# Kernel optimization log

Measured on AMD Instinct MI355X. Metric: run time of the kernel, lower is better.

Reference implementation:

```python
import jax, jax.numpy as jnp
import numpy as np

B, N, D, H = 4, 1024, 1024, 16
DH = D // H  # head dim = 64
SCALE = D ** (-0.5)  # scale_with_head=False -> dim**-0.5


def setup_inputs() -> dict:
    key = jax.random.key(0)
    ks = jax.random.split(key, 6)
    x = jax.random.normal(ks[0], (B, N, D), dtype=jnp.float32)
    mask = jax.random.randint(ks[1], (B, N - 1), 0, 2).astype(bool)
    Wqkv = jax.random.normal(ks[2], (D, 3 * D), dtype=jnp.float32) * (D ** -0.5)
    bqkv = jax.random.normal(ks[3], (3 * D,), dtype=jnp.float32) * 0.02
    Wout = jax.random.normal(ks[4], (D, D), dtype=jnp.float32) * (D ** -0.5)
    bout = jax.random.normal(ks[5], (D,), dtype=jnp.float32) * 0.02
    return {"x": x, "mask": mask, "Wqkv": Wqkv, "bqkv": bqkv, "Wout": Wout, "bout": bout}


def reference(x, mask, Wqkv, bqkv, Wout, bout):
    b, n, _ = x.shape
    qkv = x @ Wqkv + bqkv                      # [b, n, 3D]
    q, k, v = jnp.split(qkv, 3, axis=-1)
    split_heads = lambda t: t.reshape(b, n, H, DH).transpose(0, 2, 1, 3)  # [b,h,n,d]
    q, k, v = split_heads(q), split_heads(k), split_heads(v)
    dots = jnp.einsum('bhid,bhjd->bhij', q, k) * SCALE  # [b,h,n,n]
    mask_value = -jnp.finfo(dots.dtype).max
    # F.pad(mask.flatten(1), (1,0), value=True): prepend one True column
    m = jnp.concatenate([jnp.ones((b, 1), dtype=bool), mask], axis=1)  # [b, n]
    pair = m[:, None, :] & m[:, :, None]       # [b, n, n]
    dots = jnp.where(pair[:, None, :, :], dots, mask_value)
    attn = jax.nn.softmax(dots, axis=-1)
    out = jnp.einsum('bhij,bhjd->bhid', attn, v)
    out = out.transpose(0, 2, 1, 3).reshape(b, n, D)
    out = out @ Wout + bout                    # dropout p=0.0 -> identity
    return (out, attn)
```

## Files before the change

kernel.cpp:

```cpp
#include <hip/hip_runtime.h>
#include <stdint.h>

#define DEV static __device__ __forceinline__

typedef __attribute__((ext_vector_type(8))) __bf16 bfx8;
typedef __attribute__((ext_vector_type(4))) float f32x4;

DEV short f2bfbits(float f) {
  union { float f; unsigned u; } v; v.f = f;
  unsigned r = v.u + 0x7fffu + ((v.u >> 16) & 1u);
  return (short)(r >> 16);
}

DEV void gload_lds16(const void* g, void* lds) {
  __builtin_amdgcn_global_load_lds(
      (const __attribute__((address_space(1))) void*)g,
      (__attribute__((address_space(3))) void*)lds, 16, 0, 0);
}

__global__ void k_prep(const float* __restrict__ x, short* __restrict__ xb,
                       const int* __restrict__ mask, unsigned char* __restrict__ msk,
                       const float* __restrict__ Wqkv, short* __restrict__ wqkvT,
                       const float* __restrict__ Wout, short* __restrict__ woutT) {
  __shared__ float tile[32][33];
  int bx = blockIdx.x;
  int t = threadIdx.x;
  if (bx < 4096) {
    int i = bx * 256 + t;
    float4 v = ((const float4*)x)[i];
    union { short s[4]; uint64_t u; } o;
    o.s[0] = f2bfbits(v.x); o.s[1] = f2bfbits(v.y);
    o.s[2] = f2bfbits(v.z); o.s[3] = f2bfbits(v.w);
    ((uint64_t*)xb)[i] = o.u;
  } else if (bx < 4112) {
    int i = (bx - 4096) * 256 + t;
    int b = i >> 10, n = i & 1023;
    msk[i] = (n == 0) ? (unsigned char)1 : (unsigned char)(mask[b * 1023 + n - 1] != 0);
  } else {
    int tb = bx - 4112;
    int bxx = tb & 127, byy = tb >> 7;
    const float* src; short* dst; int C;
    if (bxx < 96) { src = Wqkv; dst = wqkvT; C = 3072; }
    else          { src = Wout; dst = woutT; C = 1024; bxx -= 96; }
    const int R = 1024;
    int c0 = bxx * 32, r0 = byy * 32;
    int tx = t & 31, ty = t >> 5;
    #pragma unroll
    for (int j = 0; j < 32; j += 8)
      tile[ty + j][tx] = src[(size_t)(r0 + ty + j) * C + c0 + tx];
    __syncthreads();
    #pragma unroll
    for (int j = 0; j < 32; j += 8)
      dst[(size_t)(c0 + ty + j) * R + r0 + tx] = f2bfbits(tile[tx][ty + j]);
  }
}

__global__ __launch_bounds__(256)
void k_gemm(const short* __restrict__ A, const short* __restrict__ Bt,
            const float* __restrict__ bias, int K,
            short* __restrict__ qf, short* __restrict__ kf,
            short* __restrict__ vf) {
  __shared__ short smem[8192];
  short* As = smem;
  short* Bs = smem + 4096;
  const int t = threadIdx.x;
  const int l = t & 63, w = t >> 6;
  const int lr = l & 15, lk = l >> 4;
  const int m0 = blockIdx.y * 128, n0 = blockIdx.x * 128;
  const int wr = (w >> 1) * 64, wc = (w & 1) * 64;
  f32x4 acc[4][4] = {};

  const int srow = t >> 2;
  const int sc8 = (t & 3) * 8;
  const size_t aoff1 = (size_t)(m0 + srow) * K + sc8;
  const size_t aoff2 = (size_t)(m0 + srow + 64) * K + sc8;
  const size_t boff1 = (size_t)(n0 + srow) * K + sc8;
  const size_t boff2 = (size_t)(n0 + srow + 64) * K + sc8;
  short* asd1 = As + (t & ~63) * 8;
  short* asd2 = As + (t & ~63) * 8 + 2048;
  short* bsd1 = Bs + (t & ~63) * 8;
  short* bsd2 = Bs + (t & ~63) * 8 + 2048;

  for (int k0 = 0; k0 < K; k0 += 32) {
    gload_lds16(A + aoff1 + k0, asd1);
    gload_lds16(A + aoff2 + k0, asd2);
    gload_lds16(Bt + boff1 + k0, bsd1);
    gload_lds16(Bt + boff2 + k0, bsd2);
    __syncthreads();
    bfx8 af[4], bf[4];
    #pragma unroll
    for (int m = 0; m < 4; m++)
      af[m] = *(const bfx8*)&As[(wr + m * 16 + lr) * 32 + lk * 8];
    #pragma unroll
    for (int n = 0; n < 4; n++)
      bf[n] = *(const bfx8*)&Bs[(wc + n * 16 + lr) * 32 + lk * 8];
    #pragma unroll
    for (int m = 0; m < 4; m++)
      #pragma unroll
      for (int n = 0; n < 4; n++)
        acc[m][n] = __builtin_amdgcn_mfma_f32_16x16x32_bf16(af[m], bf[n], acc[m][n], 0, 0, 0);
    __syncthreads();
  }

  const int which = n0 >> 10;
  const int head = w & 1;
  const int band = w >> 1;
  const int bb = m0 >> 10;
  const int bh = bb * 16 + ((n0 & 1023) >> 6) + head;
  short* dstp = (which == 0) ? qf : (which == 1) ? kf : vf;

  #pragma unroll
  for (int p = 0; p < 2; p++) {
    #pragma unroll
    for (int mm = 0; mm < 2; mm++) {
      int m = 2 * p + mm;
      #pragma unroll
      for (int n = 0; n < 4; n++) {
        int gc = n0 + wc + n * 16 + lr;
        float bv = bias[gc];
        #pragma unroll
        for (int i = 0; i < 4; i++) {
          short val = f2bfbits(acc[m][n][i] + bv);
          int off;
          if (which < 2) {
            off = ((((band * 2 + head) * 2 + mm) * 2 + (n >> 1)) * 64 +
                   ((2 * n + (lr >> 3)) & 3) * 16 + 4 * lk + i) * 8 + (lr & 7);
          } else {
            off = (((band * 2 + head) * 4 + n) * 64 +
                   (2 * mm + ((4 * lk + i) >> 3)) * 16 + lr) * 8 + ((4 * lk + i) & 7);
          }
          smem[off] = val;
        }
      }
    }
    __syncthreads();
    if (which < 2) {
      #pragma unroll
      for (int r = 0; r < 4; r++) {
        int rb = r >> 1, rh = r & 1;
        int bh_r = bb * 16 + ((n0 & 1023) >> 6) + rh;
        int blk0 = ((m0 & 1023) >> 4) + 4 * rb + 2 * p;
        size_t g = ((size_t)(bh_r * 64 + blk0) << 10) + t * 8;
        *(int4*)&dstp[g] = *(const int4*)&smem[r * 2048 + t * 8];
      }
    } else {
      #pragma unroll
      for (int r = 0; r < 4; r++) {
        int rb = r >> 1, rh = r & 1;
        int bh_r = bb * 16 + ((n0 & 1023) >> 6) + rh;
        int jj = ((m0 & 1023) >> 5) + 2 * rb + p;
        int db = t >> 6;
        size_t g = (((size_t)(bh_r * 4 + db) * 32 + jj) << 9) + (t & 63) * 8;
        *(int4*)&dstp[g] = *(const int4*)&smem[r * 2048 + t * 8];
      }
    }
    if (p == 0) __syncthreads();
  }
}

__global__ __launch_bounds__(256)
void k_gemm_out(const short* __restrict__ A, const short* __restrict__ Bt,
                const float* __restrict__ bias, float* __restrict__ outF) {
  __shared__ short As[128 * 32];
  __shared__ short Bs[64 * 32];
  const int K = 1024;
  const int t = threadIdx.x;
  const int l = t & 63, w = t >> 6;
  const int lr = l & 15, lk = l >> 4;
  const int m0 = blockIdx.y * 128, n0 = blockIdx.x * 64;
  const int wr = (w >> 1) * 64, wc = (w & 1) * 32;
  f32x4 acc[4][2] = {};

  const int srow = t >> 2;
  const int sc8 = (t & 3) * 8;
  const size_t aoff1 = (size_t)(m0 + srow) * K + sc8;
  const size_t aoff2 = (size_t)(m0 + srow + 64) * K + sc8;
  const size_t boff1 = (size_t)(n0 + srow) * K + sc8;
  short* asd1 = As + (t & ~63) * 8;
  short* asd2 = As + (t & ~63) * 8 + 2048;
  short* bsd1 = Bs + (t & ~63) * 8;

  for (int k0 = 0; k0 < K; k0 += 32) {
    gload_lds16(A + aoff1 + k0, asd1);
    gload_lds16(A + aoff2 + k0, asd2);
    gload_lds16(Bt + boff1 + k0, bsd1);
    __syncthreads();
    bfx8 af[4], bf[2];
    #pragma unroll
    for (int m = 0; m < 4; m++)
      af[m] = *(const bfx8*)&As[(wr + m * 16 + lr) * 32 + lk * 8];
    #pragma unroll
    for (int n = 0; n < 2; n++)
      bf[n] = *(const bfx8*)&Bs[(wc + n * 16 + lr) * 32 + lk * 8];
    #pragma unroll
    for (int m = 0; m < 4; m++)
      #pragma unroll
      for (int n = 0; n < 2; n++)
        acc[m][n] = __builtin_amdgcn_mfma_f32_16x16x32_bf16(af[m], bf[n], acc[m][n], 0, 0, 0);
    __syncthreads();
  }

  #pragma unroll
  for (int m = 0; m < 4; m++) {
    #pragma unroll
    for (int n = 0; n < 2; n++) {
      int gc = n0 + wc + n * 16 + lr;
      float bv = bias[gc];
      #pragma unroll
      for (int i = 0; i < 4; i++) {
        int gr = m0 + wr + m * 16 + 4 * lk + i;
        outF[(size_t)gr * 1024 + gc] = acc[m][n][i] + bv;
      }
    }
  }
}

__global__ __launch_bounds__(512, 4)
void k_attn(const short* __restrict__ qf_, const short* __restrict__ kf_,
            const short* __restrict__ vf_, const unsigned char* __restrict__ msk,
            float* __restrict__ attn, short* __restrict__ ctx) {
  __shared__ short P[16 * 1024];
  __shared__ float redM[16][8];
  __shared__ float redS[16][8];
  __shared__ f32x4 redC[256];
  const int t = threadIdx.x, l = t & 63, w = t >> 6;
  const int lr = l & 15, lk = l >> 4;
  const int wg = ((blockIdx.x & 7) << 9) | (blockIdx.x >> 3);
  const int rt = wg & 63, h = (wg >> 6) & 15, b = wg >> 10;
  const int bh = b * 16 + h;
  const int r0 = rt * 16;
  const float NEG = -3.402823466e38f;

  const short* qf = qf_ + ((size_t)(bh * 64 + rt) << 10);
  bfx8 aq0 = *(const bfx8*)&qf[l * 8];
  bfx8 aq1 = *(const bfx8*)&qf[512 + l * 8];

  const unsigned char* mb = msk + b * 1024;
  const bool rowok = mb[r0 + lr] != 0;

  f32x4 sc[8];
  #pragma unroll
  for (int cc = 0; cc < 8; cc++) {
    const short* kfp = kf_ + ((size_t)(bh * 64 + w * 8 + cc) << 10);
    bfx8 bk0 = *(const bfx8*)&kfp[l * 8];
    bfx8 bk1 = *(const bfx8*)&kfp[512 + l * 8];
    f32x4 a = {};
    a = __builtin_amdgcn_mfma_f32_16x16x32_bf16(bk0, aq0, a, 0, 0, 0);
    a = __builtin_amdgcn_mfma_f32_16x16x32_bf16(bk1, aq1, a, 0, 0, 0);
    unsigned cm = *(const unsigned*)&mb[w * 128 + cc * 16 + 4 * lk];
    #pragma unroll
    for (int i = 0; i < 4; i++) {
      bool ok = rowok && (((cm >> (8 * i)) & 0xffu) != 0u);
      sc[cc][i] = ok ? a[i] * 0.03125f : NEG;
    }
  }

  float m = NEG;
  #pragma unroll
  for (int f = 0; f < 8; f++)
    #pragma unroll
    for (int i = 0; i < 4; i++) m = fmaxf(m, sc[f][i]);
  m = fmaxf(m, __shfl_xor(m, 16));
  m = fmaxf(m, __shfl_xor(m, 32));
  if (lk == 0) redM[lr][w] = m;
  __syncthreads();
  {
    float4 m0 = *(const float4*)&redM[lr][0];
    float4 m1 = *(const float4*)&redM[lr][4];
    m = fmaxf(fmaxf(fmaxf(m0.x, m0.y), fmaxf(m0.z, m0.w)),
              fmaxf(fmaxf(m1.x, m1.y), fmaxf(m1.z, m1.w)));
  }
  float s = 0.f;
  #pragma unroll
  for (int f = 0; f < 8; f++)
    #pragma unroll
    for (int i = 0; i < 4; i++) { sc[f][i] = __expf(sc[f][i] - m); s += sc[f][i]; }
  s += __shfl_xor(s, 16);
  s += __shfl_xor(s, 32);
  if (lk == 0) redS[lr][w] = s;
  __syncthreads();
  float inv;
  {
    float4 s0 = *(const float4*)&redS[lr][0];
    float4 s1 = *(const float4*)&redS[lr][4];
    inv = 1.0f / (s0.x + s0.y + s0.z + s0.w + s1.x + s1.y + s1.z + s1.w);
  }

  #pragma unroll
  for (int cc = 0; cc < 8; cc++) {
    union { ushort u[4]; uint2 d; } pk;
    pk.u[0] = (ushort)f2bfbits(sc[cc][0] * inv);
    pk.u[1] = (ushort)f2bfbits(sc[cc][1] * inv);
    pk.u[2] = (ushort)f2bfbits(sc[cc][2] * inv);
    pk.u[3] = (ushort)f2bfbits(sc[cc][3] * inv);
    int slot_lin = w * 16 + cc * 2 + (lk >> 1);
    int addr = lr * 2048 + ((slot_lin ^ (lr & 7)) << 4) + ((lk & 1) << 3);
    *(uint2*)((char*)P + addr) = pk.d;
  }
  __syncthreads();

  #pragma unroll
  for (int rg = 0; rg < 2; rg++) {
    int row = w * 2 + rg;
    float* arow = attn + ((size_t)bh * 1024 + r0 + row) * 1024;
    int swr = row & 7;
    #pragma unroll
    for (int it = 0; it < 4; it++) {
      int ci = it * 64 + l;
      uint2 d = *(const uint2*)((const char*)P + row * 2048 +
                                (((ci >> 1) ^ swr) << 4) + ((ci & 1) << 3));
      float4 o;
      o.x = __uint_as_float(d.x << 16);
      o.y = __uint_as_float(d.x & 0xffff0000u);
      o.z = __uint_as_float(d.y << 16);
      o.w = __uint_as_float(d.y & 0xffff0000u);
      *(float4*)&arow[ci * 4] = o;
    }
  }

  const int dg = w & 3, ch = w >> 2;
  f32x4 o0 = {}, o1 = {};
  #pragma unroll
  for (int j = 0; j < 16; j++) {
    int jj = ch * 16 + j;
    const short* vfp = vf_ + (((size_t)(bh * 4 + dg) * 32 + jj) << 9);
    bfx8 bv = *(const bfx8*)&vfp[l * 8];
    int slot_lin = jj * 4 + lk;
    bfx8 pa = *(const bfx8*)((const char*)P + lr * 2048 +
                             ((slot_lin ^ (lr & 7)) << 4));
    if (j & 1) o1 = __builtin_amdgcn_mfma_f32_16x16x32_bf16(pa, bv, o1, 0, 0, 0);
    else       o0 = __builtin_amdgcn_mfma_f32_16x16x32_bf16(pa, bv, o0, 0, 0, 0);
  }

  f32x4 oo;
  #pragma unroll
  for (int i = 0; i < 4; i++) oo[i] = o0[i] + o1[i];
  if (w >= 4) redC[(w - 4) * 64 + l] = oo;
  __syncthreads();
  if (w < 4) {
    f32x4 op = redC[w * 64 + l];
    #pragma unroll
    for (int i = 0; i < 4; i++) {
      float v = oo[i] + op[i];
      ctx[(((size_t)b << 10) + r0 + 4 * lk + i) * 1024 + (h << 6) + (w << 4) + lr] =
          f2bfbits(v);
    }
  }
}


extern "C" void kernel_launch(void* const* d_in, const int* in_sizes, int n_in,
                              void* d_out, int out_size, void* d_ws, size_t ws_size,
                              hipStream_t stream) {
  const float* x    = (const float*)d_in[0];
  const int*   mask = (const int*)d_in[1];
  const float* Wqkv = (const float*)d_in[2];
  const float* bqkv = (const float*)d_in[3];
  const float* Wout = (const float*)d_in[4];
  const float* bout = (const float*)d_in[5];
  float* out  = (float*)d_out;
  float* attn = out + (size_t)4 * 1024 * 1024;

  char* ws = (char*)d_ws;
  short* xb    = (short*)(ws);
  short* wqkvT = (short*)(ws + 8388608);
  short* woutT = (short*)(ws + 14680064);
  short* qfr   = (short*)(ws + 16777216);
  short* kfr   = (short*)(ws + 25165824);
  short* vfr   = (short*)(ws + 33554432);
  short* ctx   = (short*)(ws + 41943040);
  unsigned char* msk = (unsigned char*)(ws + 50331648);

  k_prep<<<8208, 256, 0, stream>>>(x, xb, mask, msk, Wqkv, wqkvT, Wout, woutT);
  k_gemm<<<dim3(24, 32), 256, 0, stream>>>(xb, wqkvT, bqkv, 1024, qfr, kfr, vfr);
  k_attn<<<4096, 512, 0, stream>>>(qfr, kfr, vfr, msk, attn, ctx);
  k_gemm_out<<<dim3(16, 32), 256, 0, stream>>>(ctx, woutT, bout, out);
}
```

Measured before the change: 144.5 us.

## Process 32 query rows per attention block to reuse K/V loads

Each attention workgroup now handles two 16-row query tiles instead of one, so every K fragment loaded feeds two MFMA chains. The PV stage splits warps by row block rather than by key half, which removes the cross-warp LDS reduction of context partials and one barrier. The grid is halved, LDS for P doubles to 64KB, and launch bounds drop to 2 blocks per CU. That lowers occupancy and raises register pressure in exchange for halving K/V global traffic.

```diff
diff --git a/kernel.cpp b/kernel.cpp
--- a/kernel.cpp
+++ b/kernel.cpp
@@ -106,7 +106,6 @@
   const int head = w & 1;
   const int band = w >> 1;
   const int bb = m0 >> 10;
-  const int bh = bb * 16 + ((n0 & 1023) >> 6) + head;
   short* dstp = (which == 0) ? qf : (which == 1) ? kf : vf;
 
   #pragma unroll
@@ -215,93 +214,116 @@
   }
 }
 
-__global__ __launch_bounds__(512, 4)
+__global__ __launch_bounds__(512, 2)
 void k_attn(const short* __restrict__ qf_, const short* __restrict__ kf_,
             const short* __restrict__ vf_, const unsigned char* __restrict__ msk,
             float* __restrict__ attn, short* __restrict__ ctx) {
-  __shared__ short P[16 * 1024];
-  __shared__ float redM[16][8];
-  __shared__ float redS[16][8];
-  __shared__ f32x4 redC[256];
+  __shared__ short P[32 * 1024];
+  __shared__ float redM[32][8];
+  __shared__ float redS[32][8];
   const int t = threadIdx.x, l = t & 63, w = t >> 6;
   const int lr = l & 15, lk = l >> 4;
-  const int wg = ((blockIdx.x & 7) << 9) | (blockIdx.x >> 3);
-  const int rt = wg & 63, h = (wg >> 6) & 15, b = wg >> 10;
+  const int wg = ((blockIdx.x & 7) << 8) | (blockIdx.x >> 3);
+  const int rt = wg & 31, h = (wg >> 5) & 15, b = wg >> 9;
   const int bh = b * 16 + h;
-  const int r0 = rt * 16;
+  const int r0 = rt * 32;
   const float NEG = -3.402823466e38f;
 
-  const short* qf = qf_ + ((size_t)(bh * 64 + rt) << 10);
-  bfx8 aq0 = *(const bfx8*)&qf[l * 8];
-  bfx8 aq1 = *(const bfx8*)&qf[512 + l * 8];
+  const short* qf = qf_ + ((size_t)(bh * 64 + rt * 2) << 10);
+  bfx8 aq00 = *(const bfx8*)&qf[l * 8];
+  bfx8 aq01 = *(const bfx8*)&qf[512 + l * 8];
+  bfx8 aq10 = *(const bfx8*)&qf[1024 + l * 8];
+  bfx8 aq11 = *(const bfx8*)&qf[1536 + l * 8];
 
   const unsigned char* mb = msk + b * 1024;
-  const bool rowok = mb[r0 + lr] != 0;
-
-  f32x4 sc[8];
+  const bool rowok0 = mb[r0 + lr] != 0;
+  const bool rowok1 = mb[r0 + 16 + lr] != 0;
+
+  f32x4 sc[2][8];
   #pragma unroll
   for (int cc = 0; cc < 8; cc++) {
     const short* kfp = kf_ + ((size_t)(bh * 64 + w * 8 + cc) << 10);
     bfx8 bk0 = *(const bfx8*)&kfp[l * 8];
     bfx8 bk1 = *(const bfx8*)&kfp[512 + l * 8];
-    f32x4 a = {};
-    a = __builtin_amdgcn_mfma_f32_16x16x32_bf16(bk0, aq0, a, 0, 0, 0);
-    a = __builtin_amdgcn_mfma_f32_16x16x32_bf16(bk1, aq1, a, 0, 0, 0);
+    f32x4 a0 = {}, a1 = {};
+    a0 = __builtin_amdgcn_mfma_f32_16x16x32_bf16(bk0, aq00, a0, 0, 0, 0);
+    a0 = __builtin_amdgcn_mfma_f32_16x16x32_bf16(bk1, aq01, a0, 0, 0, 0);
+    a1 = __builtin_amdgcn_mfma_f32_16x16x32_bf16(bk0, aq10, a1, 0, 0, 0);
+    a1 = __builtin_amdgcn_mfma_f32_16x16x32_bf16(bk1, aq11, a1, 0, 0, 0);
     unsigned cm = *(const unsigned*)&mb[w * 128 + cc * 16 + 4 * lk];
     #pragma unroll
     for (int i = 0; i < 4; i++) {
-      bool ok = rowok && (((cm >> (8 * i)) & 0xffu) != 0u);
-      sc[cc][i] = ok ? a[i] * 0.03125f : NEG;
-    }
-  }
-
-  float m = NEG;
+      bool cok = ((cm >> (8 * i)) & 0xffu) != 0u;
+      sc[0][cc][i] = (cok && rowok0) ? a0[i] * 0.03125f : NEG;
+      sc[1][cc][i] = (cok && rowok1) ? a1[i] * 0.03125f : NEG;
+    }
+  }
+
+  float m0r = NEG, m1r = NEG;
   #pragma unroll
   for (int f = 0; f < 8; f++)
     #pragma unroll
-    for (int i = 0; i < 4; i++) m = fmaxf(m, sc[f][i]);
-  m = fmaxf(m, __shfl_xor(m, 16));
-  m = fmaxf(m, __shfl_xor(m, 32));
-  if (lk == 0) redM[lr][w] = m;
+    for (int i = 0; i < 4; i++) {
+      m0r = fmaxf(m0r, sc[0][f][i]);
+      m1r = fmaxf(m1r, sc[1][f][i]);
+    }
+  m0r = fmaxf(m0r, __shfl_xor(m0r, 16)); m0r = fmaxf(m0r, __shfl_xor(m0r, 32));
+  m1r = fmaxf(m1r, __shfl_xor(m1r, 16)); m1r = fmaxf(m1r, __shfl_xor(m1r, 32));
+  if (lk == 0) { redM[lr][w] = m0r; redM[16 + lr][w] = m1r; }
   __syncthreads();
   {
-    float4 m0 = *(const float4*)&redM[lr][0];
-    float4 m1 = *(const float4*)&redM[lr][4];
-    m = fmaxf(fmaxf(fmaxf(m0.x, m0.y), fmaxf(m0.z, m0.w)),
-              fmaxf(fmaxf(m1.x, m1.y), fmaxf(m1.z, m1.w)));
-  }
-  float s = 0.f;
+    float4 a = *(const float4*)&redM[lr][0];
+    float4 bq = *(const float4*)&redM[lr][4];
+    m0r = fmaxf(fmaxf(fmaxf(a.x, a.y), fmaxf(a.z, a.w)),
+                fmaxf(fmaxf(bq.x, bq.y), fmaxf(bq.z, bq.w)));
+    float4 c = *(const float4*)&redM[16 + lr][0];
+    float4 d = *(const float4*)&redM[16 + lr][4];
+    m1r = fmaxf(fmaxf(fmaxf(c.x, c.y), fmaxf(c.z, c.w)),
+                fmaxf(fmaxf(d.x, d.y), fmaxf(d.z, d.w)));
+  }
+  float s0 = 0.f, s1 = 0.f;
   #pragma unroll
   for (int f = 0; f < 8; f++)
     #pragma unroll
-    for (int i = 0; i < 4; i++) { sc[f][i] = __expf(sc[f][i] - m); s += sc[f][i]; }
-  s += __shfl_xor(s, 16);
-  s += __shfl_xor(s, 32);
-  if (lk == 0) redS[lr][w] = s;
+    for (int i = 0; i < 4; i++) {
+      sc[0][f][i] = __expf(sc[0][f][i] - m0r); s0 += sc[0][f][i];
+      sc[1][f][i] = __expf(sc[1][f][i] - m1r); s1 += sc[1][f][i];
+    }
+  s0 += __shfl_xor(s0, 16); s0 += __shfl_xor(s0, 32);
+  s1 += __shfl_xor(s1, 16); s1 += __shfl_xor(s1, 32);
+  if (lk == 0) { redS[lr][w] = s0; redS[16 + lr][w] = s1; }
   __syncthreads();
-  float inv;
+  float inv0, inv1;
   {
-    float4 s0 = *(const float4*)&redS[lr][0];
-    float4 s1 = *(const float4*)&redS[lr][4];
-    inv = 1.0f / (s0.x + s0.y + s0.z + s0.w + s1.x + s1.y + s1.z + s1.w);
-  }
-
-  #pragma unroll
-  for (int cc = 0; cc < 8; cc++) {
-    union { ushort u[4]; uint2 d; } pk;
-    pk.u[0] = (ushort)f2bfbits(sc[cc][0] * inv);
-    pk.u[1] = (ushort)f2bfbits(sc[cc][1] * inv);
-    pk.u[2] = (ushort)f2bfbits(sc[cc][2] * inv);
-    pk.u[3] = (ushort)f2bfbits(sc[cc][3] * inv);
-    int slot_lin = w * 16 + cc * 2 + (lk >> 1);
-    int addr = lr * 2048 + ((slot_lin ^ (lr & 7)) << 4) + ((lk & 1) << 3);
-    *(uint2*)((char*)P + addr) = pk.d;
+    float4 a = *(const float4*)&redS[lr][0];
+    float4 bq = *(const float4*)&redS[lr][4];
+    inv0 = 1.0f / (a.x + a.y + a.z + a.w + bq.x + bq.y + bq.z + bq.w);
+    float4 c = *(const float4*)&redS[16 + lr][0];
+    float4 d = *(const float4*)&redS[16 + lr][4];
+    inv1 = 1.0f / (c.x + c.y + c.z + c.w + d.x + d.y + d.z + d.w);
+  }
+
+  #pragma unroll
+  for (int qb = 0; qb < 2; qb++) {
+    float invq = qb ? inv1 : inv0;
+    int row = qb * 16 + lr;
+    #pragma unroll
+    for (int cc = 0; cc < 8; cc++) {
+      union { ushort u[4]; uint2 d; } pk;
+      pk.u[0] = (ushort)f2bfbits(sc[qb][cc][0] * invq);
+      pk.u[1] = (ushort)f2bfbits(sc[qb][cc][1] * invq);
+      pk.u[2] = (ushort)f2bfbits(sc[qb][cc][2] * invq);
+      pk.u[3] = (ushort)f2bfbits(sc[qb][cc][3] * invq);
+      int slot_lin = w * 16 + cc * 2 + (lk >> 1);
+      int addr = row * 2048 + ((slot_lin ^ (row & 7)) << 4) + ((lk & 1) << 3);
+      *(uint2*)((char*)P + addr) = pk.d;
+    }
   }
   __syncthreads();
 
   #pragma unroll
-  for (int rg = 0; rg < 2; rg++) {
-    int row = w * 2 + rg;
+  for (int rg = 0; rg < 4; rg++) {
+    int row = w * 4 + rg;
     float* arow = attn + ((size_t)bh * 1024 + r0 + row) * 1024;
     int swr = row & 7;
     #pragma unroll
@@ -318,33 +340,25 @@
     }
   }
 
-  const int dg = w & 3, ch = w >> 2;
+  const int dg = w & 3, rb = w >> 2;
+  const int prow = rb * 16 + lr;
+  const int psw = lr & 7;
   f32x4 o0 = {}, o1 = {};
   #pragma unroll
-  for (int j = 0; j < 16; j++) {
-    int jj = ch * 16 + j;
+  for (int jj = 0; jj < 32; jj++) {
     const short* vfp = vf_ + (((size_t)(bh * 4 + dg) * 32 + jj) << 9);
     bfx8 bv = *(const bfx8*)&vfp[l * 8];
     int slot_lin = jj * 4 + lk;
-    bfx8 pa = *(const bfx8*)((const char*)P + lr * 2048 +
-                             ((slot_lin ^ (lr & 7)) << 4));
-    if (j & 1) o1 = __builtin_amdgcn_mfma_f32_16x16x32_bf16(pa, bv, o1, 0, 0, 0);
-    else       o0 = __builtin_amdgcn_mfma_f32_16x16x32_bf16(pa, bv, o0, 0, 0, 0);
-  }
-
-  f32x4 oo;
-  #pragma unroll
-  for (int i = 0; i < 4; i++) oo[i] = o0[i] + o1[i];
-  if (w >= 4) redC[(w - 4) * 64 + l] = oo;
-  __syncthreads();
-  if (w < 4) {
-    f32x4 op = redC[w * 64 + l];
-    #pragma unroll
-    for (int i = 0; i < 4; i++) {
-      float v = oo[i] + op[i];
-      ctx[(((size_t)b << 10) + r0 + 4 * lk + i) * 1024 + (h << 6) + (w << 4) + lr] =
-          f2bfbits(v);
-    }
+    bfx8 pa = *(const bfx8*)((const char*)P + prow * 2048 +
+                             ((slot_lin ^ psw) << 4));
+    if (jj & 1) o1 = __builtin_amdgcn_mfma_f32_16x16x32_bf16(pa, bv, o1, 0, 0, 0);
+    else        o0 = __builtin_amdgcn_mfma_f32_16x16x32_bf16(pa, bv, o0, 0, 0, 0);
+  }
+  #pragma unroll
+  for (int i = 0; i < 4; i++) {
+    float v = o0[i] + o1[i];
+    ctx[(((size_t)b << 10) + r0 + rb * 16 + 4 * lk + i) * 1024 +
+        (h << 6) + (dg << 4) + lr] = f2bfbits(v);
   }
 }
 
@@ -373,6 +387,6 @@
 
   k_prep<<<8208, 256, 0, stream>>>(x, xb, mask, msk, Wqkv, wqkvT, Wout, woutT);
   k_gemm<<<dim3(24, 32), 256, 0, stream>>>(xb, wqkvT, bqkv, 1024, qfr, kfr, vfr);
-  k_attn<<<4096, 512, 0, stream>>>(qfr, kfr, vfr, msk, attn, ctx);
+  k_attn<<<2048, 512, 0, stream>>>(qfr, kfr, vfr, msk, attn, ctx);
   k_gemm_out<<<dim3(16, 32), 256, 0, stream>>>(ctx, woutT, bout, out);
 }
```

New measurement: 142.4 us, median of 2. Within noise of the previous version (-1.5%).
